# Kernel optimization log

Hardware: AMD Instinct MI355X
Metric: run time of the kernel (lower is better)

## Reference

```python
import jax, jax.numpy as jnp
import numpy as np
import math

N, M = 100000, 12
F, NF, H = 128, 64, 8
D = F // H


def setup_inputs() -> dict:
    key = jax.random.key(0)
    ks = jax.random.split(key, 20)
    s = 0.02
    inp = {
        "atom_fea": jax.random.normal(ks[0], (N, F), jnp.float32),
        "nbr_fea": jax.random.normal(ks[1], (N, M, NF), jnp.float32),
        "nbr_fea_idx": jax.random.randint(ks[2], (N, M), 0, N, jnp.int64),
        "Wq": jax.random.normal(ks[3], (F, F), jnp.float32) * s,
        "bq": jnp.zeros((F,), jnp.float32),
        "Wk": jax.random.normal(ks[4], (F, F), jnp.float32) * s,
        "bk": jnp.zeros((F,), jnp.float32),
        "Wv": jax.random.normal(ks[5], (F, F), jnp.float32) * s,
        "bv": jnp.zeros((F,), jnp.float32),
        "Wn": jax.random.normal(ks[6], (NF, F), jnp.float32) * s,
        "bn": jnp.zeros((F,), jnp.float32),
        "Wo": jax.random.normal(ks[7], (F, F), jnp.float32) * s,
        "bo": jnp.zeros((F,), jnp.float32),
        "Wg": jax.random.normal(ks[8], (2 * F, 1), jnp.float32) * s,
        "bg": jnp.zeros((1,), jnp.float32),
        "gamma": jnp.ones((F,), jnp.float32),
        "beta": jnp.zeros((F,), jnp.float32),
    }
    return inp


def reference(atom_fea, nbr_fea, nbr_fea_idx, Wq, bq, Wk, bk, Wv, bv,
              Wn, bn, Wo, bo, Wg, bg, gamma, beta):
    residual = atom_fea
    # projections [N, F] -> [N, H, D]
    q = (atom_fea @ Wq + bq).reshape(N, H, D)
    k = (atom_fea @ Wk + bk).reshape(N, H, D)
    v = (atom_fea @ Wv + bv).reshape(N, H, D)
    # gather neighbor K/V: [N, M, H, D]
    nbr_t = (nbr_fea @ Wn + bn).reshape(N, M, H, D)
    nk = k[nbr_fea_idx] + nbr_t
    nv = v[nbr_fea_idx] + nbr_t
    # scores over neighbors, per head
    scores = jnp.einsum("nhd,nmhd->nmh", q, nk) / math.sqrt(D)
    w = jax.nn.softmax(scores, axis=1)  # softmax over M neighbors
    att = jnp.einsum("nmh,nmhd->nhd", w, nv).reshape(N, F)
    out = att @ Wo + bo
    gate = jax.nn.sigmoid(jnp.concatenate([out, residual], axis=-1) @ Wg + bg)
    out = gate * out + (1.0 - gate) * residual
    # layer norm (eps=1e-5, torch default)
    mu = jnp.mean(out, axis=-1, keepdims=True)
    var = jnp.var(out, axis=-1, keepdims=True)
    out = (out - mu) * jax.lax.rsqrt(var + 1e-5) * gamma + beta
    return out
```

## Files before the change

kernel.cpp:

```cpp
#include <hip/hip_runtime.h>
#include <math.h>

#define NATOM 100000
#define MNBR 12
#define FDIM 128
#define NFDIM 64

typedef __attribute__((ext_vector_type(8))) short bf16x8;
typedef __attribute__((ext_vector_type(4))) float f32x4;
typedef unsigned short u16;

__device__ inline u16 f2bf(float x) {
    union { float f; unsigned u; } v; v.f = x;
    unsigned r = v.u + 0x7FFFu + ((v.u >> 16) & 1u);
    return (u16)(r >> 16);
}

__device__ inline float b2f(u16 u) {
    union { unsigned u; float f; } v; v.u = ((unsigned)u) << 16;
    return v.f;
}

__device__ inline void st4bf(short* p, float4 x) {
    unsigned lo = (unsigned)f2bf(x.x) | ((unsigned)f2bf(x.y) << 16);
    unsigned hi = (unsigned)f2bf(x.z) | ((unsigned)f2bf(x.w) << 16);
    *(uint2*)p = make_uint2(lo, hi);
}

__global__ __launch_bounds__(256) void pack_weights(
    const float* __restrict__ Wq, const float* __restrict__ Wk,
    const float* __restrict__ Wv, const float* __restrict__ Wn,
    const float* __restrict__ Wo,
    short* __restrict__ pk1, short* __restrict__ pk2, short* __restrict__ pk3)
{
    int g = blockIdx.x * 256 + threadIdx.x;
    if (g < 49152) {
        int fe = g >> 9;
        int r = g & 511;
        int lane = r >> 3, jj = r & 7;
        int s = fe & 3, f = fe >> 2;
        int ct = f & 7, mt = f >> 3;
        int k = s * 32 + (lane >> 4) * 8 + jj;
        int n = ct * 16 + (lane & 15);
        const float* W = (mt == 0) ? Wq : ((mt == 1) ? Wk : Wv);
        pk1[g] = (short)f2bf(W[k * 128 + n]);
    } else if (g < 57344) {
        int g2 = g - 49152;
        int fe = g2 >> 9;
        int r = g2 & 511;
        int lane = r >> 3, jj = r & 7;
        int s = fe & 1, ct = fe >> 1;
        int k = s * 32 + (lane >> 4) * 8 + jj;
        int n = ct * 16 + (lane & 15);
        pk2[g2] = (short)f2bf(Wn[k * 128 + n]);
    } else {
        int g3 = g - 57344;
        int fe = g3 >> 9;
        int r = g3 & 511;
        int lane = r >> 3, jj = r & 7;
        int s = fe & 3, ct = fe >> 2;
        int k = s * 32 + (lane >> 4) * 8 + jj;
        int n = ct * 16 + (lane & 15);
        pk3[g3] = (short)f2bf(Wo[k * 128 + n]);
    }
}

__global__ __launch_bounds__(256) void qkv_mfma(
    const float* __restrict__ atom_fea,
    const short* __restrict__ pk1,
    const float* __restrict__ bq, const float* __restrict__ bk,
    const float* __restrict__ bv,
    u16* __restrict__ q, u16* __restrict__ k, u16* __restrict__ v)
{
    __shared__ short s_a[128 * 136];
    const int tid = threadIdx.x;
    const int base = blockIdx.x * 128;
#pragma unroll
    for (int e = 0; e < 16; ++e) {
        int f4 = e * 256 + tid;
        int row = f4 >> 5, c4 = f4 & 31;
        int atom = base + row;
        float4 x = make_float4(0.f, 0.f, 0.f, 0.f);
        if (atom < NATOM) x = *(const float4*)(atom_fea + (size_t)atom * 128 + c4 * 4);
        st4bf(&s_a[row * 136 + c4 * 4], x);
    }
    __syncthreads();

    const int lane = tid & 63, w = tid >> 6;
    const int quad = lane >> 4, j16 = lane & 15;

    for (int rt = 0; rt < 8; ++rt) {
        f32x4 acc[6];
#pragma unroll
        for (int fl = 0; fl < 6; ++fl) acc[fl] = (f32x4){0.f, 0.f, 0.f, 0.f};

        const short* arow = &s_a[(rt * 16 + j16) * 136];
#pragma unroll
        for (int s = 0; s < 4; ++s) {
            bf16x8 af = *(const bf16x8*)(arow + s * 32 + quad * 8);
            bf16x8 bfr[6];
#pragma unroll
            for (int fl = 0; fl < 6; ++fl)
                bfr[fl] = *(const bf16x8*)(pk1 + ((((w * 6 + fl) * 4 + s) * 64 + lane) << 3));
#pragma unroll
            for (int fl = 0; fl < 6; ++fl)
                acc[fl] = __builtin_amdgcn_mfma_f32_16x16x32_bf16(af, bfr[fl], acc[fl], 0, 0, 0);
        }
#pragma unroll
        for (int fl = 0; fl < 6; ++fl) {
            const int f = w * 6 + fl;
            const int mt = f >> 3, ct = f & 7;
            const int col = ct * 16 + j16;
            const float b = (mt == 0 ? bq : (mt == 1 ? bk : bv))[col];
            u16* op = (mt == 0 ? q : (mt == 1 ? k : v));
#pragma unroll
            for (int r = 0; r < 4; ++r) {
                int atom = base + rt * 16 + quad * 4 + r;
                if (atom < NATOM) op[(unsigned)atom * 128u + col] = f2bf(acc[fl][r] + b);
            }
        }
    }
}

__global__ __launch_bounds__(256) void attn_mfma(
    const float* __restrict__ nbr_fea,
    const int*   __restrict__ nbr_idx,
    const short* __restrict__ pk2,
    const float* __restrict__ bn,
    u16* qatt,
    const u16* __restrict__ kbuf,
    const u16* __restrict__ vbuf)
{
    __shared__ short s_a[8 * 16 * 72];
    __shared__ u16   s_q[8 * 128];
    const int tid = threadIdx.x;
    const long long blk = blockIdx.x;

    const float* gsrc = nbr_fea + blk * 6144;
#pragma unroll
    for (int e = 0; e < 6; ++e) {
        int f4 = e * 256 + tid;
        int r = f4 >> 4, c4 = f4 & 15;
        int a = r / 12, m = r - a * 12;
        int lrow = (m / 3) * 4 + (m % 3);
        float4 x = *(const float4*)(gsrc + (size_t)f4 * 4);
        st4bf(&s_a[(a * 16 + lrow) * 72 + c4 * 4], x);
    }
    {
        int prow = tid >> 3, c = tid & 7;
        int a = prow >> 2, qd = prow & 3;
        *(uint4*)&s_a[(a * 16 + qd * 4 + 3) * 72 + c * 8] = make_uint4(0, 0, 0, 0);
    }
    if (tid < 128) {
        ((uint4*)s_q)[tid] = ((const uint4*)(qatt + (size_t)blk * 1024))[tid];
    }
    __syncthreads();

    const int lane = tid & 63, w = tid >> 6;
    const int quad = lane >> 4, j16 = lane & 15;

    bf16x8 bfr[2][2];
#pragma unroll
    for (int hh = 0; hh < 2; ++hh)
#pragma unroll
        for (int s = 0; s < 2; ++s) {
            int ct = w * 2 + hh;
            bfr[hh][s] = *(const bf16x8*)(pk2 + (((ct * 2 + s) * 64 + lane) << 3));
        }

    const float bnc0 = bn[w * 32 + j16];
    const float bnc1 = bn[w * 32 + 16 + j16];
    const unsigned base8 = (unsigned)blk * 8u;
    const int cb = w * 32 + j16;

#pragma unroll
    for (int a = 0; a < 8; ++a) {
        const unsigned n = base8 + a;
        int nidx[3];
#pragma unroll
        for (int r = 0; r < 3; ++r)
            nidx[r] = nbr_idx[n * 12u + quad * 3 + r];

        f32x4 acc0 = (f32x4){0.f, 0.f, 0.f, 0.f};
        f32x4 acc1 = (f32x4){0.f, 0.f, 0.f, 0.f};
#pragma unroll
        for (int s = 0; s < 2; ++s) {
            bf16x8 af = *(const bf16x8*)&s_a[(a * 16 + j16) * 72 + s * 32 + quad * 8];
            acc0 = __builtin_amdgcn_mfma_f32_16x16x32_bf16(af, bfr[0][s], acc0, 0, 0, 0);
            acc1 = __builtin_amdgcn_mfma_f32_16x16x32_bf16(af, bfr[1][s], acc1, 0, 0, 0);
        }

        unsigned off[3];
#pragma unroll
        for (int r = 0; r < 3; ++r) off[r] = ((unsigned)nidx[r]) << 7;

        float kk[2][3], vv[2][3];
#pragma unroll
        for (int hh = 0; hh < 2; ++hh) {
            const int c = cb + hh * 16;
#pragma unroll
            for (int r = 0; r < 3; ++r) {
                kk[hh][r] = b2f(kbuf[off[r] + c]);
                vv[hh][r] = b2f(vbuf[off[r] + c]);
            }
        }

#pragma unroll
        for (int hh = 0; hh < 2; ++hh) {
            const int c = cb + hh * 16;
            const float qv = b2f(s_q[a * 128 + c]);
            const float bnc = hh ? bnc1 : bnc0;
            const f32x4 t = hh ? acc1 : acc0;
            float sc[3], nv[3];
#pragma unroll
            for (int r = 0; r < 3; ++r) {
                float tm = t[r] + bnc;
                float nk = kk[hh][r] + tm;
                nv[r] = vv[hh][r] + tm;
                float p = qv * nk;
                p += __shfl_xor(p, 1, 16);
                p += __shfl_xor(p, 2, 16);
                p += __shfl_xor(p, 4, 16);
                p += __shfl_xor(p, 8, 16);
                sc[r] = p * 0.25f;
            }
            float mx = fmaxf(fmaxf(sc[0], sc[1]), sc[2]);
            mx = fmaxf(mx, __shfl_xor(mx, 16));
            mx = fmaxf(mx, __shfl_xor(mx, 32));
            float es = 0.f, av = 0.f;
#pragma unroll
            for (int r = 0; r < 3; ++r) {
                float e = __expf(sc[r] - mx);
                es += e;
                av += e * nv[r];
            }
            es += __shfl_xor(es, 16); es += __shfl_xor(es, 32);
            av += __shfl_xor(av, 16); av += __shfl_xor(av, 32);
            if (quad == 0) qatt[n * 128u + c] = f2bf(av * __builtin_amdgcn_rcpf(es));
        }
    }
}

__global__ __launch_bounds__(256) void out_mfma(
    const u16* __restrict__ attb, const float* __restrict__ atom_fea,
    const short* __restrict__ pk3, const float* __restrict__ bo,
    const float* __restrict__ Wg, const float* __restrict__ bg,
    const float* __restrict__ gamma, const float* __restrict__ beta,
    float* __restrict__ out)
{
    __shared__ short s_a[64 * 136];
    __shared__ float s_o[64 * 132];
    const int tid = threadIdx.x;
    const int base = blockIdx.x * 64;
#pragma unroll
    for (int e = 0; e < 4; ++e) {
        int u = e * 256 + tid;
        int row = u >> 4, c8 = u & 15;
        int atom = base + row;
        uint4 x = make_uint4(0, 0, 0, 0);
        if (atom < NATOM) x = *(const uint4*)(attb + (size_t)atom * 128 + c8 * 8);
        *(uint4*)&s_a[row * 136 + c8 * 8] = x;
    }
    __syncthreads();

    const int lane = tid & 63, w = tid >> 6;
    const int quad = lane >> 4, j16 = lane & 15;

    f32x4 acc[8];
#pragma unroll
    for (int f = 0; f < 8; ++f) acc[f] = (f32x4){0.f, 0.f, 0.f, 0.f};

    const short* arow = &s_a[(w * 16 + j16) * 136];
#pragma unroll
    for (int s = 0; s < 4; ++s) {
        bf16x8 af = *(const bf16x8*)(arow + s * 32 + quad * 8);
        bf16x8 bfr[8];
#pragma unroll
        for (int f = 0; f < 8; ++f)
            bfr[f] = *(const bf16x8*)(pk3 + (((f * 4 + s) * 64 + lane) << 3));
#pragma unroll
        for (int f = 0; f < 8; ++f)
            acc[f] = __builtin_amdgcn_mfma_f32_16x16x32_bf16(af, bfr[f], acc[f], 0, 0, 0);
    }
#pragma unroll
    for (int f = 0; f < 8; ++f) {
        const int col = f * 16 + j16;
        const float b = bo[col];
#pragma unroll
        for (int r = 0; r < 4; ++r)
            s_o[(w * 16 + quad * 4 + r) * 132 + col] = acc[f][r] + b;
    }
    __syncthreads();

    const int g = tid >> 4;
    const int r16 = tid & 15;
    for (int p = 0; p < 4; ++p) {
        const int a_loc = p * 16 + g;
        const int atom = base + a_loc;
        const bool ok = (atom < NATOM);
        float o8[8], res8[8];
        float pg = 0.f;
#pragma unroll
        for (int tt = 0; tt < 8; ++tt) {
            int jj = r16 + tt * 16;
            o8[tt] = s_o[a_loc * 132 + jj];
            res8[tt] = ok ? atom_fea[(size_t)atom * 128 + jj] : 0.f;
            pg += o8[tt] * Wg[jj] + res8[tt] * Wg[128 + jj];
        }
        pg += __shfl_xor(pg, 1, 16);
        pg += __shfl_xor(pg, 2, 16);
        pg += __shfl_xor(pg, 4, 16);
        pg += __shfl_xor(pg, 8, 16);
        const float gt = 1.f / (1.f + __expf(-(pg + bg[0])));

        float s1 = 0.f, s2 = 0.f;
        float gv8[8];
#pragma unroll
        for (int tt = 0; tt < 8; ++tt) {
            float gv = gt * o8[tt] + (1.f - gt) * res8[tt];
            gv8[tt] = gv;
            s1 += gv; s2 += gv * gv;
        }
        s1 += __shfl_xor(s1, 1, 16); s2 += __shfl_xor(s2, 1, 16);
        s1 += __shfl_xor(s1, 2, 16); s2 += __shfl_xor(s2, 2, 16);
        s1 += __shfl_xor(s1, 4, 16); s2 += __shfl_xor(s2, 4, 16);
        s1 += __shfl_xor(s1, 8, 16); s2 += __shfl_xor(s2, 8, 16);
        const float mu = s1 * (1.f / 128.f);
        const float var = s2 * (1.f / 128.f) - mu * mu;
        const float rs = rsqrtf(var + 1e-5f);
        if (ok) {
#pragma unroll
            for (int tt = 0; tt < 8; ++tt) {
                int jj = r16 + tt * 16;
                out[(size_t)atom * 128 + jj] =
                    (gv8[tt] - mu) * rs * gamma[jj] + beta[jj];
            }
        }
    }
}

extern "C" void kernel_launch(void* const* d_in, const int* in_sizes, int n_in,
                              void* d_out, int out_size, void* d_ws, size_t ws_size,
                              hipStream_t stream) {
    const float* atom_fea = (const float*)d_in[0];
    const float* nbr_fea  = (const float*)d_in[1];
    const int*   nbr_idx  = (const int*)d_in[2];
    const float* Wq = (const float*)d_in[3];
    const float* bq = (const float*)d_in[4];
    const float* Wk = (const float*)d_in[5];
    const float* bk = (const float*)d_in[6];
    const float* Wv = (const float*)d_in[7];
    const float* bv = (const float*)d_in[8];
    const float* Wn = (const float*)d_in[9];
    const float* bn = (const float*)d_in[10];
    const float* Wo = (const float*)d_in[11];
    const float* bo = (const float*)d_in[12];
    const float* Wg = (const float*)d_in[13];
    const float* bg = (const float*)d_in[14];
    const float* gm = (const float*)d_in[15];
    const float* bt = (const float*)d_in[16];

    u16* qbuf = (u16*)d_ws;
    u16* kbuf = qbuf + (size_t)NATOM * FDIM;
    u16* vbuf = kbuf + (size_t)NATOM * FDIM;
    short* pk1 = (short*)(vbuf + (size_t)NATOM * FDIM);
    short* pk2 = pk1 + 49152;
    short* pk3 = pk2 + 8192;
    float* outp = (float*)d_out;

    pack_weights<<<288, 256, 0, stream>>>(Wq, Wk, Wv, Wn, Wo, pk1, pk2, pk3);
    qkv_mfma<<<(NATOM + 127) / 128, 256, 0, stream>>>(
        atom_fea, pk1, bq, bk, bv, qbuf, kbuf, vbuf);
    attn_mfma<<<NATOM / 8, 256, 0, stream>>>(
        nbr_fea, nbr_idx, pk2, bn, qbuf, kbuf, vbuf);
    out_mfma<<<(NATOM + 63) / 64, 256, 0, stream>>>(
        qbuf, atom_fea, pk3, bo, Wg, bg, gm, bt, outp);
}
```

Baseline: 667.0 us.

## Stage neighbor K/V gathers into LDS via global_load_lds per atom

Neighbor indices are preloaded into registers once per block. For each atom, one wave issues direct global-to-LDS 16-byte loads of the 12 gathered K and V rows into a shared staging buffer. All waves then read from LDS instead of each lane doing scattered 2-byte global loads. This cuts the number of gather instructions and widens each access. In exchange it adds two block barriers per atom and uses a single staging buffer, so each atom's gather latency is only partly hidden behind the previous atom's compute.

```diff
diff --git a/kernel.cpp b/kernel.cpp
--- a/kernel.cpp
+++ b/kernel.cpp
@@ -131,8 +131,9 @@
     const u16* __restrict__ kbuf,
     const u16* __restrict__ vbuf)
 {
-    __shared__ short s_a[8 * 16 * 72];
-    __shared__ u16   s_q[8 * 128];
+    __shared__ __align__(16) short s_a[8 * 16 * 72];
+    __shared__ __align__(16) u16   s_q[8 * 128];
+    __shared__ __align__(16) u16   s_kv[6 * 528];
     const int tid = threadIdx.x;
     const long long blk = blockIdx.x;
 
@@ -154,10 +155,19 @@
     if (tid < 128) {
         ((uint4*)s_q)[tid] = ((const uint4*)(qatt + (size_t)blk * 1024))[tid];
     }
-    __syncthreads();
 
     const int lane = tid & 63, w = tid >> 6;
     const int quad = lane >> 4, j16 = lane & 15;
+    const unsigned base8 = (unsigned)blk * 8u;
+
+    int nid[2][3];
+#pragma unroll
+    for (int s = 0; s < 2; ++s)
+#pragma unroll
+        for (int r = 0; r < 3; ++r)
+            nid[s][r] = nbr_idx[(base8 + w + 4 * s) * 12u + r * 4 + quad];
+
+    __syncthreads();
 
     bf16x8 bfr[2][2];
 #pragma unroll
@@ -170,16 +180,26 @@
 
     const float bnc0 = bn[w * 32 + j16];
     const float bnc1 = bn[w * 32 + 16 + j16];
-    const unsigned base8 = (unsigned)blk * 8u;
     const int cb = w * 32 + j16;
+    const int lchunk = (lane & 15) << 3;
+
+    auto issue = [&](int a, int s) {
+#pragma unroll
+        for (int j = 0; j < 6; ++j) {
+            const int r = (j >= 3) ? (j - 3) : j;
+            const u16* src = ((j >= 3) ? vbuf : kbuf)
+                + (((size_t)(unsigned)nid[s][r]) << 7) + lchunk;
+            __builtin_amdgcn_global_load_lds(
+                (const __attribute__((address_space(1))) void*)src,
+                (__attribute__((address_space(3))) void*)((char*)s_kv + j * 1056),
+                16, 0, 0);
+        }
+    };
+    if (w == 0) issue(0, 0);
 
 #pragma unroll
     for (int a = 0; a < 8; ++a) {
         const unsigned n = base8 + a;
-        int nidx[3];
-#pragma unroll
-        for (int r = 0; r < 3; ++r)
-            nidx[r] = nbr_idx[n * 12u + quad * 3 + r];
 
         f32x4 acc0 = (f32x4){0.f, 0.f, 0.f, 0.f};
         f32x4 acc1 = (f32x4){0.f, 0.f, 0.f, 0.f};
@@ -190,20 +210,7 @@
             acc1 = __builtin_amdgcn_mfma_f32_16x16x32_bf16(af, bfr[1][s], acc1, 0, 0, 0);
         }
 
-        unsigned off[3];
-#pragma unroll
-        for (int r = 0; r < 3; ++r) off[r] = ((unsigned)nidx[r]) << 7;
-
-        float kk[2][3], vv[2][3];
-#pragma unroll
-        for (int hh = 0; hh < 2; ++hh) {
-            const int c = cb + hh * 16;
-#pragma unroll
-            for (int r = 0; r < 3; ++r) {
-                kk[hh][r] = b2f(kbuf[off[r] + c]);
-                vv[hh][r] = b2f(vbuf[off[r] + c]);
-            }
-        }
+        __syncthreads();
 
 #pragma unroll
         for (int hh = 0; hh < 2; ++hh) {
@@ -214,9 +221,13 @@
             float sc[3], nv[3];
 #pragma unroll
             for (int r = 0; r < 3; ++r) {
+                const int m = quad * 3 + r;
+                const int mk = m, mv = m + 12;
+                float kkv = b2f(s_kv[(mk >> 2) * 528 + (mk & 3) * 128 + c]);
+                float vvv = b2f(s_kv[(mv >> 2) * 528 + (mv & 3) * 128 + c]);
                 float tm = t[r] + bnc;
-                float nk = kk[hh][r] + tm;
-                nv[r] = vv[hh][r] + tm;
+                float nk = kkv + tm;
+                nv[r] = vvv + tm;
                 float p = qv * nk;
                 p += __shfl_xor(p, 1, 16);
                 p += __shfl_xor(p, 2, 16);
@@ -238,6 +249,9 @@
             av += __shfl_xor(av, 16); av += __shfl_xor(av, 32);
             if (quad == 0) qatt[n * 128u + c] = f2bf(av * __builtin_amdgcn_rcpf(es));
         }
+
+        __syncthreads();
+        if (a < 7 && w == ((a + 1) & 3)) issue(a + 1, (a + 1) >> 2);
     }
 }
 
```

New measurement: 678.7 us. Within noise of the previous version (+1.8%).

## Vectorize neighbor K/V gathers to bf16 pairs and hoist index/weight loads

Applied to the files above, without the earlier changes.

The attention kernel now handles two adjacent columns per lane. It reads K, V, q and Wn fragments as packed 32-bit bf16 pairs, with the Wn packing permuted to match, and the score reduction drops one shuffle stage. All neighbor indices are loaded up front and overlapped with the shared-memory staging barrier, and the QKV kernel preloads its full weight fragments into registers before the barrier. This is meant to halve gather transactions and hide index and weight load latency, at the cost of higher register pressure.

```diff
diff --git a/kernel.cpp b/kernel.cpp
--- a/kernel.cpp
+++ b/kernel.cpp
@@ -19,6 +19,13 @@
 __device__ inline float b2f(u16 u) {
     union { unsigned u; float f; } v; v.u = ((unsigned)u) << 16;
     return v.f;
+}
+
+__device__ inline float bflo(unsigned w) {
+    union { unsigned u; float f; } v; v.u = w << 16; return v.f;
+}
+__device__ inline float bfhi(unsigned w) {
+    union { unsigned u; float f; } v; v.u = w & 0xffff0000u; return v.f;
 }
 
 __device__ inline void st4bf(short* p, float4 x) {
@@ -51,7 +58,7 @@
         int lane = r >> 3, jj = r & 7;
         int s = fe & 1, ct = fe >> 1;
         int k = s * 32 + (lane >> 4) * 8 + jj;
-        int n = ct * 16 + (lane & 15);
+        int n = (ct >> 1) * 32 + ((lane & 15) << 1) + (ct & 1);
         pk2[g2] = (short)f2bf(Wn[k * 128 + n]);
     } else {
         int g3 = g - 57344;
@@ -84,11 +91,19 @@
         if (atom < NATOM) x = *(const float4*)(atom_fea + (size_t)atom * 128 + c4 * 4);
         st4bf(&s_a[row * 136 + c4 * 4], x);
     }
-    __syncthreads();
 
     const int lane = tid & 63, w = tid >> 6;
     const int quad = lane >> 4, j16 = lane & 15;
 
+    bf16x8 bfr[6][4];
+#pragma unroll
+    for (int fl = 0; fl < 6; ++fl)
+#pragma unroll
+        for (int s = 0; s < 4; ++s)
+            bfr[fl][s] = *(const bf16x8*)(pk1 + ((((w * 6 + fl) * 4 + s) * 64 + lane) << 3));
+
+    __syncthreads();
+
     for (int rt = 0; rt < 8; ++rt) {
         f32x4 acc[6];
 #pragma unroll
@@ -98,13 +113,9 @@
 #pragma unroll
         for (int s = 0; s < 4; ++s) {
             bf16x8 af = *(const bf16x8*)(arow + s * 32 + quad * 8);
-            bf16x8 bfr[6];
 #pragma unroll
             for (int fl = 0; fl < 6; ++fl)
-                bfr[fl] = *(const bf16x8*)(pk1 + ((((w * 6 + fl) * 4 + s) * 64 + lane) << 3));
-#pragma unroll
-            for (int fl = 0; fl < 6; ++fl)
-                acc[fl] = __builtin_amdgcn_mfma_f32_16x16x32_bf16(af, bfr[fl], acc[fl], 0, 0, 0);
+                acc[fl] = __builtin_amdgcn_mfma_f32_16x16x32_bf16(af, bfr[fl][s], acc[fl], 0, 0, 0);
         }
 #pragma unroll
         for (int fl = 0; fl < 6; ++fl) {
@@ -131,8 +142,8 @@
     const u16* __restrict__ kbuf,
     const u16* __restrict__ vbuf)
 {
-    __shared__ short s_a[8 * 16 * 72];
-    __shared__ u16   s_q[8 * 128];
+    __shared__ __align__(16) short s_a[8 * 16 * 72];
+    __shared__ __align__(16) u16   s_q[8 * 128];
     const int tid = threadIdx.x;
     const long long blk = blockIdx.x;
 
@@ -154,10 +165,20 @@
     if (tid < 128) {
         ((uint4*)s_q)[tid] = ((const uint4*)(qatt + (size_t)blk * 1024))[tid];
     }
-    __syncthreads();
 
     const int lane = tid & 63, w = tid >> 6;
     const int quad = lane >> 4, j16 = lane & 15;
+    const unsigned base8 = (unsigned)blk * 8u;
+
+    unsigned voff[8][3];
+#pragma unroll
+    for (int a = 0; a < 8; ++a)
+#pragma unroll
+        for (int r = 0; r < 3; ++r)
+            voff[a][r] = ((unsigned)nbr_idx[(base8 + a) * 12u + quad * 3 + r]) * 64u
+                         + (unsigned)(w * 16 + j16);
+
+    __syncthreads();
 
     bf16x8 bfr[2][2];
 #pragma unroll
@@ -168,18 +189,18 @@
             bfr[hh][s] = *(const bf16x8*)(pk2 + (((ct * 2 + s) * 64 + lane) << 3));
         }
 
-    const float bnc0 = bn[w * 32 + j16];
-    const float bnc1 = bn[w * 32 + 16 + j16];
-    const unsigned base8 = (unsigned)blk * 8u;
-    const int cb = w * 32 + j16;
+    const float2 bnc = *(const float2*)(bn + w * 32 + 2 * j16);
+    const unsigned* kptr = (const unsigned*)kbuf;
+    const unsigned* vptr = (const unsigned*)vbuf;
 
 #pragma unroll
     for (int a = 0; a < 8; ++a) {
-        const unsigned n = base8 + a;
-        int nidx[3];
-#pragma unroll
-        for (int r = 0; r < 3; ++r)
-            nidx[r] = nbr_idx[n * 12u + quad * 3 + r];
+        unsigned kw[3], vw[3];
+#pragma unroll
+        for (int r = 0; r < 3; ++r) {
+            kw[r] = kptr[voff[a][r]];
+            vw[r] = vptr[voff[a][r]];
+        }
 
         f32x4 acc0 = (f32x4){0.f, 0.f, 0.f, 0.f};
         f32x4 acc1 = (f32x4){0.f, 0.f, 0.f, 0.f};
@@ -190,53 +211,43 @@
             acc1 = __builtin_amdgcn_mfma_f32_16x16x32_bf16(af, bfr[1][s], acc1, 0, 0, 0);
         }
 
-        unsigned off[3];
-#pragma unroll
-        for (int r = 0; r < 3; ++r) off[r] = ((unsigned)nidx[r]) << 7;
-
-        float kk[2][3], vv[2][3];
-#pragma unroll
-        for (int hh = 0; hh < 2; ++hh) {
-            const int c = cb + hh * 16;
-#pragma unroll
-            for (int r = 0; r < 3; ++r) {
-                kk[hh][r] = b2f(kbuf[off[r] + c]);
-                vv[hh][r] = b2f(vbuf[off[r] + c]);
-            }
-        }
-
-#pragma unroll
-        for (int hh = 0; hh < 2; ++hh) {
-            const int c = cb + hh * 16;
-            const float qv = b2f(s_q[a * 128 + c]);
-            const float bnc = hh ? bnc1 : bnc0;
-            const f32x4 t = hh ? acc1 : acc0;
-            float sc[3], nv[3];
-#pragma unroll
-            for (int r = 0; r < 3; ++r) {
-                float tm = t[r] + bnc;
-                float nk = kk[hh][r] + tm;
-                nv[r] = vv[hh][r] + tm;
-                float p = qv * nk;
-                p += __shfl_xor(p, 1, 16);
-                p += __shfl_xor(p, 2, 16);
-                p += __shfl_xor(p, 4, 16);
-                p += __shfl_xor(p, 8, 16);
-                sc[r] = p * 0.25f;
-            }
-            float mx = fmaxf(fmaxf(sc[0], sc[1]), sc[2]);
-            mx = fmaxf(mx, __shfl_xor(mx, 16));
-            mx = fmaxf(mx, __shfl_xor(mx, 32));
-            float es = 0.f, av = 0.f;
-#pragma unroll
-            for (int r = 0; r < 3; ++r) {
-                float e = __expf(sc[r] - mx);
-                es += e;
-                av += e * nv[r];
-            }
-            es += __shfl_xor(es, 16); es += __shfl_xor(es, 32);
-            av += __shfl_xor(av, 16); av += __shfl_xor(av, 32);
-            if (quad == 0) qatt[n * 128u + c] = f2bf(av * __builtin_amdgcn_rcpf(es));
+        unsigned qw = *(const unsigned*)&s_q[a * 128 + w * 32 + 2 * j16];
+        const float q0 = bflo(qw), q1 = bfhi(qw);
+
+        float sc[3], nv0[3], nv1[3];
+#pragma unroll
+        for (int r = 0; r < 3; ++r) {
+            float tm0 = acc0[r] + bnc.x;
+            float tm1 = acc1[r] + bnc.y;
+            float k0 = bflo(kw[r]) + tm0;
+            float k1 = bfhi(kw[r]) + tm1;
+            nv0[r] = bflo(vw[r]) + tm0;
+            nv1[r] = bfhi(vw[r]) + tm1;
+            float p = q0 * k0 + q1 * k1;
+            p += __shfl_xor(p, 1, 16);
+            p += __shfl_xor(p, 2, 16);
+            p += __shfl_xor(p, 4, 16);
+            sc[r] = p * 0.25f;
+        }
+        float mx = fmaxf(fmaxf(sc[0], sc[1]), sc[2]);
+        mx = fmaxf(mx, __shfl_xor(mx, 16));
+        mx = fmaxf(mx, __shfl_xor(mx, 32));
+        float es = 0.f, av0 = 0.f, av1 = 0.f;
+#pragma unroll
+        for (int r = 0; r < 3; ++r) {
+            float e = __expf(sc[r] - mx);
+            es += e;
+            av0 += e * nv0[r];
+            av1 += e * nv1[r];
+        }
+        es  += __shfl_xor(es, 16);  es  += __shfl_xor(es, 32);
+        av0 += __shfl_xor(av0, 16); av0 += __shfl_xor(av0, 32);
+        av1 += __shfl_xor(av1, 16); av1 += __shfl_xor(av1, 32);
+        if (quad == 0) {
+            float rs = __builtin_amdgcn_rcpf(es);
+            unsigned pr = (unsigned)f2bf(av0 * rs)
+                        | ((unsigned)f2bf(av1 * rs) << 16);
+            *(unsigned*)&qatt[(base8 + a) * 128u + w * 32 + 2 * j16] = pr;
         }
     }
 }
```

New measurement: 598.2 us. -10.3%, faster.
